# Kernel tuning notes

Hardware: AMD Instinct MI355X
Metric: run time of the kernel (lower is better)

Reference implementation:

```python
import jax, jax.numpy as jnp
import numpy as np

EMB = 128
EA = 32
ET = 32
N = 50000
E = 500000
EPS = 1e-5
DROP_P = 0.1


def setup_inputs() -> dict:
    key = jax.random.key(0)
    ks = jax.random.split(key, 12)
    din = EMB + EA + ET
    return {
        "hidden": jax.random.normal(ks[0], (N, EMB), jnp.float32),
        "edge_index": jax.random.randint(ks[1], (2, E), 0, N, jnp.int64 if jax.config.jax_enable_x64 else jnp.int32),
        "edge_attr": jax.random.normal(ks[2], (E, EA), jnp.float32),
        "edge_time_emb": jax.random.normal(ks[3], (E, ET), jnp.float32),
        "boundary_condition": jax.random.normal(ks[4], (N, EMB), jnp.float32),
        # learned params (torch Linear stored transposed: [in, out])
        "W_msg": jax.random.normal(ks[5], (din, EMB), jnp.float32) / np.sqrt(din),
        "b_msg": jnp.zeros((EMB,), jnp.float32),
        "W_lin": jax.random.normal(ks[6], (EMB, EMB), jnp.float32) / np.sqrt(EMB),
        "b_lin": jnp.zeros((EMB,), jnp.float32),
        "ln_gamma": jnp.ones((EMB,), jnp.float32),
        "ln_beta": jnp.zeros((EMB,), jnp.float32),
    }


def reference(hidden, edge_index, edge_attr, edge_time_emb, boundary_condition,
              W_msg, b_msg, W_lin, b_lin, ln_gamma, ln_beta):
    num_nodes = hidden.shape[0]
    # gather source node features, concat with edge features -> [E, emb+ea+et]
    msg = jnp.concatenate([hidden[edge_index[0]], edge_attr, edge_time_emb], axis=1)
    msg = jax.nn.relu(msg @ W_msg + b_msg)                      # [E, emb]
    # append boundary condition as self-loop messages
    msg_aug = jnp.concatenate([msg, boundary_condition], axis=0)
    idx_aug = jnp.concatenate([edge_index[1], jnp.arange(num_nodes, dtype=edge_index.dtype)])
    out = jax.ops.segment_sum(msg_aug, idx_aug, num_segments=num_nodes)  # scatter-sum [N, emb]
    out = out @ W_lin + b_lin
    # LayerNorm (eps=1e-5, affine)
    mean = out.mean(-1, keepdims=True)
    var = out.var(-1, keepdims=True)
    out = (out - mean) * jax.lax.rsqrt(var + EPS) * ln_gamma + ln_beta
    out = jax.nn.relu(out)
    # dropout p=0.1, training=True (fixed key for reproducibility)
    keep = jax.random.bernoulli(jax.random.key(42), 1.0 - DROP_P, out.shape)
    out = jnp.where(keep, out / (1.0 - DROP_P), 0.0)
    return out
```

## Files before the change

kernel.cpp:

```cpp
#include <hip/hip_runtime.h>
#include <stdint.h>

#define NN 50000
#define NE 500000
#define NEPAD 500032
#define SPB 64
#define NT_BLOCKS ((NN + 63) / 64)
#define DEG_STRIDE (NT_BLOCKS * 256)
#define NBLK_N ((NN + 255) / 256)

typedef short bf16x8 __attribute__((ext_vector_type(8)));
typedef float f32x4 __attribute__((ext_vector_type(4)));
typedef unsigned short u16;
typedef unsigned short u16x4 __attribute__((ext_vector_type(4)));
typedef unsigned short u16x8 __attribute__((ext_vector_type(8)));
typedef unsigned int u32x4 __attribute__((ext_vector_type(4)));

__device__ __forceinline__ u16 f2b(float x) {
  uint32_t u = __builtin_bit_cast(uint32_t, x);
  return (u16)((u + 0x7fffu + ((u >> 16) & 1u)) >> 16);
}
__device__ __forceinline__ float b2f(uint32_t lo16) {
  return __builtin_bit_cast(float, lo16 << 16);
}

__device__ __forceinline__ void threefry(uint32_t x0, uint32_t x1,
                                         uint32_t& o0, uint32_t& o1) {
  const uint32_t k0 = 0u, k1 = 42u, k2 = 0u ^ 42u ^ 0x1BD11BDAu;
  x0 += k0; x1 += k1;
#define TFR(r) { x0 += x1; x1 = (x1 << r) | (x1 >> (32 - r)); x1 ^= x0; }
  TFR(13) TFR(15) TFR(26) TFR(6)
  x0 += k1; x1 += k2 + 1u;
  TFR(17) TFR(29) TFR(16) TFR(24)
  x0 += k2; x1 += k0 + 2u;
  TFR(13) TFR(15) TFR(26) TFR(6)
  x0 += k0; x1 += k1 + 3u;
  TFR(17) TFR(29) TFR(16) TFR(24)
  x0 += k1; x1 += k2 + 4u;
  TFR(13) TFR(15) TFR(26) TFR(6)
  x0 += k2; x1 += k0 + 5u;
#undef TFR
  o0 = x0; o1 = x1;
}

__device__ __forceinline__ bool jax_keep(uint32_t j) {
  uint32_t o0, o1;
  threefry(0u, j, o0, o1);
  uint32_t bits = o0 ^ o1;
  float u = __builtin_bit_cast(float, (bits >> 9) | 0x3f800000u) - 1.0f;
  return u < 0.9f;
}

__global__ __launch_bounds__(256) void k_prep(const float* __restrict__ Wmsg,
                                              const float* __restrict__ Wlin,
                                              u16* __restrict__ WhImg,
                                              u16* __restrict__ WcImg,
                                              u16* __restrict__ WlImg) {
  const int t = threadIdx.x, b = blockIdx.x;
  if (b == 0) {
#pragma unroll
    for (int it = 0; it < 16; ++it) {
      int g = t + (it << 8);
      int d = g >> 5, k4 = (g & 31) << 2;
      u16x4 v = {f2b(Wmsg[(k4 + 0) * 128 + d]), f2b(Wmsg[(k4 + 1) * 128 + d]),
                 f2b(Wmsg[(k4 + 2) * 128 + d]), f2b(Wmsg[(k4 + 3) * 128 + d])};
      *(u16x4*)&WhImg[(d << 7) + k4] = v;
    }
  } else if (b == 1) {
#pragma unroll
    for (int it = 0; it < 8; ++it) {
      int g = t + (it << 8);
      int d = g >> 4, k4 = (g & 15) << 2;
      u16x4 v = {f2b(Wmsg[(128 + k4 + 0) * 128 + d]), f2b(Wmsg[(128 + k4 + 1) * 128 + d]),
                 f2b(Wmsg[(128 + k4 + 2) * 128 + d]), f2b(Wmsg[(128 + k4 + 3) * 128 + d])};
      *(u16x4*)&WcImg[(d << 6) + k4] = v;
    }
  } else {
#pragma unroll
    for (int it = 0; it < 16; ++it) {
      int g = t + (it << 8);
      int d = g >> 5, k4 = (g & 31) << 2;
      u16x4 v = {f2b(Wlin[(k4 + 0) * 128 + d]), f2b(Wlin[(k4 + 1) * 128 + d]),
                 f2b(Wlin[(k4 + 2) * 128 + d]), f2b(Wlin[(k4 + 3) * 128 + d])};
      *(u16x4*)&WlImg[(d << 7) + k4] = v;
    }
  }
}

__global__ __launch_bounds__(256) void k_scan1(const uint32_t* __restrict__ deg,
                                               uint32_t* __restrict__ ex,
                                               uint32_t* __restrict__ bsum) {
  __shared__ uint32_t s[256];
  int t = threadIdx.x;
  int i = blockIdx.x * 256 + t;
  uint32_t v = (i < NN) ? deg[i] : 0u;
  s[t] = v;
  __syncthreads();
#pragma unroll
  for (int off = 1; off < 256; off <<= 1) {
    uint32_t y = (t >= off) ? s[t - off] : 0u;
    __syncthreads();
    s[t] += y;
    __syncthreads();
  }
  if (i < NN) ex[i] = s[t] - v;
  if (t == 255) bsum[blockIdx.x] = s[255];
}

__global__ __launch_bounds__(256) void k_scan2(const uint32_t* __restrict__ bsum,
                                               uint32_t* __restrict__ boff) {
  __shared__ uint32_t s[256];
  int t = threadIdx.x;
  uint32_t v = (t < NBLK_N) ? bsum[t] : 0u;
  s[t] = v;
  __syncthreads();
#pragma unroll
  for (int off = 1; off < 256; off <<= 1) {
    uint32_t y = (t >= off) ? s[t - off] : 0u;
    __syncthreads();
    s[t] += y;
    __syncthreads();
  }
  boff[t] = s[t] - v;
}

__global__ __launch_bounds__(256) void k_scan3(const uint32_t* __restrict__ ex,
                                               const uint32_t* __restrict__ boff,
                                               uint32_t* __restrict__ cursor) {
  int i = blockIdx.x * 256 + threadIdx.x;
  if (i < NN) cursor[i] = ex[i] + boff[blockIdx.x];
}

__global__ __launch_bounds__(256) void k_permconv(const int* __restrict__ ei,
                                                  const float* __restrict__ attr,
                                                  const float* __restrict__ tim,
                                                  uint32_t* __restrict__ cursor,
                                                  u16* __restrict__ Abf,
                                                  int* __restrict__ perm) {
  const int t = threadIdx.x;
  const int j = t & 7;
  const long e = (long)blockIdx.x * 32 + (t >> 3);
  if (e >= NE) return;
  const float* src8 = (j < 4) ? (attr + ((size_t)e << 5) + (j << 3))
                              : (tim + ((size_t)e << 5) + ((j - 4) << 3));
  f32x4 v0 = *(const f32x4*)src8;
  f32x4 v1 = *(const f32x4*)(src8 + 4);
  u16x8 b = {f2b(v0[0]), f2b(v0[1]), f2b(v0[2]), f2b(v0[3]),
             f2b(v1[0]), f2b(v1[1]), f2b(v1[2]), f2b(v1[3])};
  *(u16x8*)&Abf[((size_t)e << 6) + (j << 3)] = b;
  if (j == 0) {
    uint32_t dst = (uint32_t)ei[NE + e];
    uint32_t pos = atomicAdd(&cursor[dst], 1u);
    perm[pos] = (int)e;
  }
}

__global__ __launch_bounds__(256, 4) void k_edge3(const int* __restrict__ perm,
                                                  const u16* __restrict__ Abf,
                                                  const int* __restrict__ ei,
                                                  const u16* __restrict__ WcImg,
                                                  const u16* __restrict__ Hp,
                                                  float* __restrict__ acc) {
  __shared__ union { u16 A[64 * 64]; float C[64 * 128]; } lds;
  __shared__ int sdst[64];
  const int t = threadIdx.x;
  const long e0 = (long)blockIdx.x << 6;

#pragma unroll
  for (int it = 0; it < 2; ++it) {
    int li = t + (it << 8);
    int row = li >> 3, g = li & 7;
    long sg = e0 + row;
    u32x4 v = {0u, 0u, 0u, 0u};
    if (sg < NE) {
      int e = perm[sg];
      v = *(const u32x4*)(Abf + ((size_t)e << 6) + (g << 3));
    }
    *(u32x4*)&lds.A[(row << 6) + ((g ^ (row & 7)) << 3)] = v;
  }
  const int s = t >> 2, q = t & 3;
  const long sg1 = e0 + s;
  const bool v1 = sg1 < NE;
  int src = 0, dstn = -1;
  if (v1) {
    int e = perm[sg1];
    src = ei[e];
    dstn = ei[NE + e];
  }
  u32x4 hp[4];
  if (v1) {
    const u32x4* hp4 = (const u32x4*)(Hp + ((size_t)src << 7) + (q << 5));
#pragma unroll
    for (int g = 0; g < 4; ++g) hp[g] = hp4[g];
  }
  if (q == 0) sdst[s] = v1 ? dstn : -1;
  __syncthreads();

  const int lane = t & 63, w = t >> 6;
  const int quad = lane >> 4, lr = lane & 15;
  f32x4 c[4][2];
#pragma unroll
  for (int i = 0; i < 4; ++i)
#pragma unroll
    for (int j = 0; j < 2; ++j) { f32x4 z = {0.f, 0.f, 0.f, 0.f}; c[i][j] = z; }
#pragma unroll
  for (int ks = 0; ks < 64; ks += 32) {
    const int gi = (ks >> 3) + quad;
    bf16x8 a[4], b[2];
#pragma unroll
    for (int i = 0; i < 4; ++i) {
      int row = (i << 4) + lr;
      a[i] = *(const bf16x8*)&lds.A[(row << 6) + ((gi ^ (row & 7)) << 3)];
    }
#pragma unroll
    for (int j = 0; j < 2; ++j) {
      int col = (w << 5) + (j << 4) + lr;
      b[j] = *(const bf16x8*)&WcImg[(col << 6) + (gi << 3)];
    }
#pragma unroll
    for (int i = 0; i < 4; ++i)
#pragma unroll
      for (int j = 0; j < 2; ++j)
        c[i][j] = __builtin_amdgcn_mfma_f32_16x16x32_bf16(a[i], b[j], c[i][j], 0, 0, 0);
  }
  __syncthreads();
#pragma unroll
  for (int i = 0; i < 4; ++i)
#pragma unroll
    for (int j = 0; j < 2; ++j)
#pragma unroll
      for (int r = 0; r < 4; ++r) {
        int row = (i << 4) + (quad << 2) + r;
        int col = (w << 5) + (j << 4) + lr;
        lds.C[(row << 7) + ((((col >> 2) ^ (row & 31)) << 2) + (col & 3))] = c[i][j][r];
      }
  __syncthreads();
  if (v1) {
#pragma unroll
    for (int g = 0; g < 8; ++g) {
      int cb = (q << 5) + (g << 2);
      float* p = &lds.C[(s << 7) + ((((cb >> 2) ^ (s & 31)) << 2))];
      f32x4 cv = *(const f32x4*)p;
      uint32_t w0 = hp[g >> 1][(g & 1) << 1];
      uint32_t w1 = hp[g >> 1][((g & 1) << 1) + 1];
      cv[0] = fmaxf(cv[0] + b2f(w0 & 0xffffu), 0.f);
      cv[1] = fmaxf(cv[1] + b2f(w0 >> 16), 0.f);
      cv[2] = fmaxf(cv[2] + b2f(w1 & 0xffffu), 0.f);
      cv[3] = fmaxf(cv[3] + b2f(w1 >> 16), 0.f);
      *(f32x4*)p = cv;
    }
  }
  __syncthreads();
  {
    const int col = t & 127, half = t >> 7;
    const int beg = half << 5, end = beg + 32;
    int cur = sdst[beg];
    float sum = 0.f;
    int runstart = beg;
    for (int ss = beg; ss < end; ++ss) {
      int d = sdst[ss];
      if (d != cur) {
        if (cur >= 0) {
          float* p = acc + ((size_t)cur << 7) + col;
          if (runstart == beg) unsafeAtomicAdd(p, sum);
          else *p = sum;
        }
        cur = d; sum = 0.f; runstart = ss;
      }
      sum += lds.C[(ss << 7) + ((((col >> 2) ^ (ss & 31)) << 2) + (col & 3))];
    }
    if (cur >= 0) unsafeAtomicAdd(acc + ((size_t)cur << 7) + col, sum);
  }
}

__global__ __launch_bounds__(256) void k_hp(const float* __restrict__ hidden,
                                            const u16* __restrict__ WhImg,
                                            const float* __restrict__ bmsg,
                                            const int* __restrict__ ei,
                                            uint32_t* __restrict__ deg,
                                            u16* __restrict__ Hp) {
  __shared__ u16 sA[64 * 128];
  const int t = threadIdx.x;
  const int row0 = blockIdx.x << 6;
  for (int i = blockIdx.x * 256 + t; i < NE; i += DEG_STRIDE)
    atomicAdd(&deg[ei[NE + i]], 1u);
#pragma unroll
  for (int it = 0; it < 8; ++it) {
    int li = t + (it << 8);
    int row = li >> 5, c4 = li & 31;
    int n = row0 + row;
    f32x4 v = {0.f, 0.f, 0.f, 0.f};
    if (n < NN) v = *(const f32x4*)(hidden + ((size_t)n << 7) + (c4 << 2));
    u16x4 b = {f2b(v[0]), f2b(v[1]), f2b(v[2]), f2b(v[3])};
    *(u16x4*)&sA[(row << 7) + ((((c4 >> 1) ^ (row & 15)) << 3) + ((c4 & 1) << 2))] = b;
  }
  __syncthreads();
  const int lane = t & 63, w = t >> 6;
  const int quad = lane >> 4, lr = lane & 15;
  f32x4 c[4][2];
#pragma unroll
  for (int i = 0; i < 4; ++i)
#pragma unroll
    for (int j = 0; j < 2; ++j) { f32x4 z = {0.f, 0.f, 0.f, 0.f}; c[i][j] = z; }
#pragma unroll
  for (int ks = 0; ks < 128; ks += 32) {
    const int gi = (ks >> 3) + quad;
    bf16x8 a[4], b[2];
#pragma unroll
    for (int i = 0; i < 4; ++i) {
      int row = (i << 4) + lr;
      a[i] = *(const bf16x8*)&sA[(row << 7) + ((gi ^ (row & 15)) << 3)];
    }
#pragma unroll
    for (int j = 0; j < 2; ++j) {
      int col = (w << 5) + (j << 4) + lr;
      b[j] = *(const bf16x8*)&WhImg[(col << 7) + (gi << 3)];
    }
#pragma unroll
    for (int i = 0; i < 4; ++i)
#pragma unroll
      for (int j = 0; j < 2; ++j)
        c[i][j] = __builtin_amdgcn_mfma_f32_16x16x32_bf16(a[i], b[j], c[i][j], 0, 0, 0);
  }
#pragma unroll
  for (int j = 0; j < 2; ++j) {
    int d = (w << 5) + (j << 4) + lr;
    float bias = bmsg[d];
#pragma unroll
    for (int i = 0; i < 4; ++i) {
      int nb = row0 + (i << 4) + (quad << 2);
#pragma unroll
      for (int r = 0; r < 4; ++r) {
        int n = nb + r;
        if (n < NN) Hp[((size_t)n << 7) + d] = f2b(c[i][j][r] + bias);
      }
    }
  }
}

__global__ __launch_bounds__(256) void k_out(float* accout,
                                             const float* __restrict__ bnd,
                                             const u16* __restrict__ WlImg,
                                             const float* __restrict__ blin,
                                             const float* __restrict__ gam,
                                             const float* __restrict__ bet) {
  __shared__ union { u16 A[64 * 128]; float C[64 * 128]; } lds;
  const int t = threadIdx.x;
  const int row0 = blockIdx.x << 6;
#pragma unroll
  for (int it = 0; it < 8; ++it) {
    int li = t + (it << 8);
    int row = li >> 5, c4 = li & 31;
    int n = row0 + row;
    f32x4 v = {0.f, 0.f, 0.f, 0.f};
    if (n < NN) {
      f32x4 a = *(const f32x4*)(accout + ((size_t)n << 7) + (c4 << 2));
      f32x4 b = *(const f32x4*)(bnd + ((size_t)n << 7) + (c4 << 2));
      v = a + b;
    }
    u16x4 bb = {f2b(v[0]), f2b(v[1]), f2b(v[2]), f2b(v[3])};
    *(u16x4*)&lds.A[(row << 7) + ((((c4 >> 1) ^ (row & 15)) << 3) + ((c4 & 1) << 2))] = bb;
  }
  __syncthreads();
  const int lane = t & 63, w = t >> 6;
  const int quad = lane >> 4, lr = lane & 15;
  f32x4 c[4][2];
#pragma unroll
  for (int i = 0; i < 4; ++i)
#pragma unroll
    for (int j = 0; j < 2; ++j) { f32x4 z = {0.f, 0.f, 0.f, 0.f}; c[i][j] = z; }
#pragma unroll
  for (int ks = 0; ks < 128; ks += 32) {
    const int gi = (ks >> 3) + quad;
    bf16x8 a[4], b[2];
#pragma unroll
    for (int i = 0; i < 4; ++i) {
      int row = (i << 4) + lr;
      a[i] = *(const bf16x8*)&lds.A[(row << 7) + ((gi ^ (row & 15)) << 3)];
    }
#pragma unroll
    for (int j = 0; j < 2; ++j) {
      int col = (w << 5) + (j << 4) + lr;
      b[j] = *(const bf16x8*)&WlImg[(col << 7) + (gi << 3)];
    }
#pragma unroll
    for (int i = 0; i < 4; ++i)
#pragma unroll
      for (int j = 0; j < 2; ++j)
        c[i][j] = __builtin_amdgcn_mfma_f32_16x16x32_bf16(a[i], b[j], c[i][j], 0, 0, 0);
  }
  __syncthreads();
#pragma unroll
  for (int i = 0; i < 4; ++i)
#pragma unroll
    for (int j = 0; j < 2; ++j)
#pragma unroll
      for (int r = 0; r < 4; ++r) {
        int row = (i << 4) + (quad << 2) + r;
        int col = (w << 5) + (j << 4) + lr;
        lds.C[(row << 7) + ((((col >> 2) ^ (row & 31)) << 2) + (col & 3))] = c[i][j][r];
      }
  __syncthreads();
  const int row = t >> 2, q = t & 3;
  const int n = row0 + row;
  float s1 = 0.f, s2 = 0.f;
  if (n < NN) {
#pragma unroll
    for (int g = 0; g < 8; ++g) {
      int g5 = (q << 3) + g;
      f32x4 cv = *(const f32x4*)&lds.C[(row << 7) + ((g5 ^ (row & 31)) << 2)];
      f32x4 bl = *(const f32x4*)(blin + (g5 << 2));
#pragma unroll
      for (int m = 0; m < 4; ++m) {
        float x = cv[m] + bl[m];
        s1 += x; s2 += x * x;
      }
    }
  }
  s1 += __shfl_xor(s1, 1, 64); s1 += __shfl_xor(s1, 2, 64);
  s2 += __shfl_xor(s2, 1, 64); s2 += __shfl_xor(s2, 2, 64);
  if (n < NN) {
    const float mean = s1 * 0.0078125f;
    const float var = s2 * 0.0078125f - mean * mean;
    const float inv = 1.0f / sqrtf(var + 1e-5f);
#pragma unroll
    for (int g = 0; g < 8; ++g) {
      int g5 = (q << 3) + g;
      int d0 = g5 << 2;
      f32x4 cv = *(const f32x4*)&lds.C[(row << 7) + ((g5 ^ (row & 31)) << 2)];
      f32x4 bl = *(const f32x4*)(blin + d0);
      f32x4 gm = *(const f32x4*)(gam + d0);
      f32x4 bb = *(const f32x4*)(bet + d0);
      f32x4 o;
#pragma unroll
      for (int m = 0; m < 4; ++m) {
        float x = cv[m] + bl[m];
        float y = fmaxf((x - mean) * inv * gm[m] + bb[m], 0.f);
        uint32_t jj = ((uint32_t)n << 7) + (uint32_t)(d0 + m);
        o[m] = jax_keep(jj) ? (y * (1.0f / 0.9f)) : 0.0f;
      }
      *(f32x4*)(accout + ((size_t)n << 7) + d0) = o;
    }
  }
}

extern "C" void kernel_launch(void* const* d_in, const int* in_sizes, int n_in,
                              void* d_out, int out_size, void* d_ws, size_t ws_size,
                              hipStream_t stream) {
  (void)in_sizes; (void)n_in; (void)out_size; (void)ws_size;
  const float* hidden = (const float*)d_in[0];
  const int*   ei     = (const int*)d_in[1];
  const float* attr   = (const float*)d_in[2];
  const float* tim    = (const float*)d_in[3];
  const float* bnd    = (const float*)d_in[4];
  const float* Wmsg   = (const float*)d_in[5];
  const float* bmsg   = (const float*)d_in[6];
  const float* Wlin   = (const float*)d_in[7];
  const float* blin   = (const float*)d_in[8];
  const float* gam    = (const float*)d_in[9];
  const float* bet    = (const float*)d_in[10];

  float* acc = (float*)d_out;

  char* ws = (char*)d_ws;
  u16*      Hp     = (u16*)(ws + 0);
  u16*      WhImg  = (u16*)(ws + 12800000);
  u16*      WcImg  = (u16*)(ws + 12832768);
  u16*      WlImg  = (u16*)(ws + 12849152);
  uint32_t* deg    = (uint32_t*)(ws + 12881920);
  uint32_t* cursor = (uint32_t*)(ws + 13081920);
  uint32_t* bsum   = (uint32_t*)(ws + 13281920);
  uint32_t* boff   = (uint32_t*)(ws + 13282944);
  uint32_t* ex     = (uint32_t*)(ws + 13283968);
  int*      perm   = (int*)(ws + 13483968);
  u16*      Abf    = (u16*)(ws + 15484096);

  hipMemsetAsync(deg, 0, (size_t)NN * 4, stream);
  hipMemsetAsync(acc, 0, (size_t)NN * 128 * 4, stream);

  k_prep <<<dim3(3), dim3(256), 0, stream>>>(Wmsg, Wlin, WhImg, WcImg, WlImg);
  k_hp   <<<dim3(NT_BLOCKS), dim3(256), 0, stream>>>(hidden, WhImg, bmsg, ei, deg, Hp);
  k_scan1<<<dim3(NBLK_N), dim3(256), 0, stream>>>(deg, ex, bsum);
  k_scan2<<<dim3(1), dim3(256), 0, stream>>>(bsum, boff);
  k_scan3<<<dim3(NBLK_N), dim3(256), 0, stream>>>(ex, boff, cursor);
  k_permconv<<<dim3(NE / 32), dim3(256), 0, stream>>>(ei, attr, tim, cursor, Abf, perm);
  k_edge3<<<dim3(NEPAD / SPB), dim3(256), 0, stream>>>(perm, Abf, ei, WcImg, Hp, acc);
  k_out  <<<dim3(NT_BLOCKS), dim3(256), 0, stream>>>(acc, bnd, WlImg, blin, gam, bet);
}
```

Baseline: 373.3 us.

## Drop bf16 edge-feature staging; gather fp32 attrs directly and pack src/dst per sorted slot

Removes the intermediate bf16 copy of the edge attribute and time features. The edge kernel now gathers the fp32 features through the permutation and converts them in registers, saving one full write and read pass over the edge features. The permutation kernel also stores a packed 16-bit src/dst pair per sorted slot, which replaces the dependent perm-then-edge_index lookups. The epilogue LDS buffer is halved by writing and reducing the 128 output columns in two halves, which should allow more blocks per CU but adds extra barriers and makes the fp32 gathers scattered instead of streaming.

```diff
diff --git a/kernel.cpp b/kernel.cpp
--- a/kernel.cpp
+++ b/kernel.cpp
@@ -131,37 +131,27 @@
   if (i < NN) cursor[i] = ex[i] + boff[blockIdx.x];
 }
 
-__global__ __launch_bounds__(256) void k_permconv(const int* __restrict__ ei,
+__global__ __launch_bounds__(256) void k_perm(const int* __restrict__ ei,
+                                              uint32_t* __restrict__ cursor,
+                                              int* __restrict__ perm,
+                                              uint32_t* __restrict__ sd) {
+  int i = blockIdx.x * 256 + threadIdx.x;
+  if (i < NE) {
+    uint32_t s = (uint32_t)ei[i], d = (uint32_t)ei[NE + i];
+    uint32_t pos = atomicAdd(&cursor[d], 1u);
+    perm[pos] = i;
+    sd[pos] = s | (d << 16);
+  }
+}
+
+__global__ __launch_bounds__(256, 4) void k_edge3(const int* __restrict__ perm,
+                                                  const uint32_t* __restrict__ sd,
                                                   const float* __restrict__ attr,
                                                   const float* __restrict__ tim,
-                                                  uint32_t* __restrict__ cursor,
-                                                  u16* __restrict__ Abf,
-                                                  int* __restrict__ perm) {
-  const int t = threadIdx.x;
-  const int j = t & 7;
-  const long e = (long)blockIdx.x * 32 + (t >> 3);
-  if (e >= NE) return;
-  const float* src8 = (j < 4) ? (attr + ((size_t)e << 5) + (j << 3))
-                              : (tim + ((size_t)e << 5) + ((j - 4) << 3));
-  f32x4 v0 = *(const f32x4*)src8;
-  f32x4 v1 = *(const f32x4*)(src8 + 4);
-  u16x8 b = {f2b(v0[0]), f2b(v0[1]), f2b(v0[2]), f2b(v0[3]),
-             f2b(v1[0]), f2b(v1[1]), f2b(v1[2]), f2b(v1[3])};
-  *(u16x8*)&Abf[((size_t)e << 6) + (j << 3)] = b;
-  if (j == 0) {
-    uint32_t dst = (uint32_t)ei[NE + e];
-    uint32_t pos = atomicAdd(&cursor[dst], 1u);
-    perm[pos] = (int)e;
-  }
-}
-
-__global__ __launch_bounds__(256, 4) void k_edge3(const int* __restrict__ perm,
-                                                  const u16* __restrict__ Abf,
-                                                  const int* __restrict__ ei,
                                                   const u16* __restrict__ WcImg,
                                                   const u16* __restrict__ Hp,
                                                   float* __restrict__ acc) {
-  __shared__ union { u16 A[64 * 64]; float C[64 * 128]; } lds;
+  __shared__ union { u16 A[64 * 64]; float C[64 * 64]; } lds;
   __shared__ int sdst[64];
   const int t = threadIdx.x;
   const long e0 = (long)blockIdx.x << 6;
@@ -171,27 +161,37 @@
     int li = t + (it << 8);
     int row = li >> 3, g = li & 7;
     long sg = e0 + row;
-    u32x4 v = {0u, 0u, 0u, 0u};
-    if (sg < NE) {
-      int e = perm[sg];
-      v = *(const u32x4*)(Abf + ((size_t)e << 6) + (g << 3));
-    }
-    *(u32x4*)&lds.A[(row << 6) + ((g ^ (row & 7)) << 3)] = v;
+    const bool vld = sg < NE;
+    int e = 0;
+    if (vld) e = perm[sg];
+    const float* src8 = (g < 4) ? (attr + ((size_t)e << 5) + (g << 3))
+                                : (tim + ((size_t)e << 5) + ((g - 4) << 3));
+    f32x4 v0 = {0.f, 0.f, 0.f, 0.f}, v1 = {0.f, 0.f, 0.f, 0.f};
+    if (vld) {
+      v0 = *(const f32x4*)src8;
+      v1 = *(const f32x4*)(src8 + 4);
+    }
+    u16x8 b = {f2b(v0[0]), f2b(v0[1]), f2b(v0[2]), f2b(v0[3]),
+               f2b(v1[0]), f2b(v1[1]), f2b(v1[2]), f2b(v1[3])};
+    *(u16x8*)&lds.A[(row << 6) + ((g ^ (row & 7)) << 3)] = b;
   }
   const int s = t >> 2, q = t & 3;
   const long sg1 = e0 + s;
   const bool v1 = sg1 < NE;
   int src = 0, dstn = -1;
   if (v1) {
-    int e = perm[sg1];
-    src = ei[e];
-    dstn = ei[NE + e];
+    uint32_t sdv = sd[sg1];
+    src = (int)(sdv & 0xffffu);
+    dstn = (int)(sdv >> 16);
   }
   u32x4 hp[4];
   if (v1) {
-    const u32x4* hp4 = (const u32x4*)(Hp + ((size_t)src << 7) + (q << 5));
-#pragma unroll
-    for (int g = 0; g < 4; ++g) hp[g] = hp4[g];
+#pragma unroll
+    for (int h = 0; h < 2; ++h)
+#pragma unroll
+      for (int k = 0; k < 2; ++k)
+        hp[(h << 1) + k] =
+            *(const u32x4*)(Hp + ((size_t)src << 7) + (h << 6) + (q << 4) + (k << 3));
   }
   if (q == 0) sdst[s] = v1 ? dstn : -1;
   __syncthreads();
@@ -224,52 +224,62 @@
         c[i][j] = __builtin_amdgcn_mfma_f32_16x16x32_bf16(a[i], b[j], c[i][j], 0, 0, 0);
   }
   __syncthreads();
-#pragma unroll
-  for (int i = 0; i < 4; ++i)
-#pragma unroll
-    for (int j = 0; j < 2; ++j)
-#pragma unroll
-      for (int r = 0; r < 4; ++r) {
-        int row = (i << 4) + (quad << 2) + r;
-        int col = (w << 5) + (j << 4) + lr;
-        lds.C[(row << 7) + ((((col >> 2) ^ (row & 31)) << 2) + (col & 3))] = c[i][j][r];
-      }
-  __syncthreads();
-  if (v1) {
-#pragma unroll
-    for (int g = 0; g < 8; ++g) {
-      int cb = (q << 5) + (g << 2);
-      float* p = &lds.C[(s << 7) + ((((cb >> 2) ^ (s & 31)) << 2))];
-      f32x4 cv = *(const f32x4*)p;
-      uint32_t w0 = hp[g >> 1][(g & 1) << 1];
-      uint32_t w1 = hp[g >> 1][((g & 1) << 1) + 1];
-      cv[0] = fmaxf(cv[0] + b2f(w0 & 0xffffu), 0.f);
-      cv[1] = fmaxf(cv[1] + b2f(w0 >> 16), 0.f);
-      cv[2] = fmaxf(cv[2] + b2f(w1 & 0xffffu), 0.f);
-      cv[3] = fmaxf(cv[3] + b2f(w1 >> 16), 0.f);
-      *(f32x4*)p = cv;
-    }
-  }
-  __syncthreads();
-  {
-    const int col = t & 127, half = t >> 7;
-    const int beg = half << 5, end = beg + 32;
-    int cur = sdst[beg];
-    float sum = 0.f;
-    int runstart = beg;
-    for (int ss = beg; ss < end; ++ss) {
-      int d = sdst[ss];
-      if (d != cur) {
-        if (cur >= 0) {
-          float* p = acc + ((size_t)cur << 7) + col;
-          if (runstart == beg) unsafeAtomicAdd(p, sum);
-          else *p = sum;
+
+#pragma unroll
+  for (int h = 0; h < 2; ++h) {
+    if ((w >> 1) == h) {
+#pragma unroll
+      for (int i = 0; i < 4; ++i)
+#pragma unroll
+        for (int j = 0; j < 2; ++j)
+#pragma unroll
+          for (int r = 0; r < 4; ++r) {
+            int row = (i << 4) + (quad << 2) + r;
+            int colh = ((w & 1) << 5) + (j << 4) + lr;
+            lds.C[(row << 6) + ((((colh >> 2) ^ (row & 15)) << 2) + (colh & 3))] =
+                c[i][j][r];
+          }
+    }
+    __syncthreads();
+    if (v1) {
+      const u32x4 h0 = hp[h << 1], h1 = hp[(h << 1) + 1];
+#pragma unroll
+      for (int g = 0; g < 4; ++g) {
+        int cb = (q << 4) + (g << 2);
+        float* p = &lds.C[(s << 6) + (((cb >> 2) ^ (s & 15)) << 2)];
+        f32x4 cv = *(const f32x4*)p;
+        u32x4 hw = (g < 2) ? h0 : h1;
+        uint32_t w0 = hw[(g & 1) << 1];
+        uint32_t w1 = hw[((g & 1) << 1) + 1];
+        cv[0] = fmaxf(cv[0] + b2f(w0 & 0xffffu), 0.f);
+        cv[1] = fmaxf(cv[1] + b2f(w0 >> 16), 0.f);
+        cv[2] = fmaxf(cv[2] + b2f(w1 & 0xffffu), 0.f);
+        cv[3] = fmaxf(cv[3] + b2f(w1 >> 16), 0.f);
+        *(f32x4*)p = cv;
+      }
+    }
+    __syncthreads();
+    {
+      const int col = t & 63, rng = t >> 6;
+      const int beg = rng << 4, end = beg + 16;
+      int cur = sdst[beg];
+      float sum = 0.f;
+      int runstart = beg;
+      for (int ss = beg; ss < end; ++ss) {
+        int d = sdst[ss];
+        if (d != cur) {
+          if (cur >= 0) {
+            float* p = acc + ((size_t)cur << 7) + (h << 6) + col;
+            if (runstart == beg) unsafeAtomicAdd(p, sum);
+            else *p = sum;
+          }
+          cur = d; sum = 0.f; runstart = ss;
         }
-        cur = d; sum = 0.f; runstart = ss;
-      }
-      sum += lds.C[(ss << 7) + ((((col >> 2) ^ (ss & 31)) << 2) + (col & 3))];
-    }
-    if (cur >= 0) unsafeAtomicAdd(acc + ((size_t)cur << 7) + col, sum);
+        sum += lds.C[(ss << 6) + ((((col >> 2) ^ (ss & 15)) << 2) + (col & 3))];
+      }
+      if (cur >= 0) unsafeAtomicAdd(acc + ((size_t)cur << 7) + (h << 6) + col, sum);
+    }
+    __syncthreads();
   }
 }
 
@@ -472,8 +482,8 @@
   uint32_t* bsum   = (uint32_t*)(ws + 13281920);
   uint32_t* boff   = (uint32_t*)(ws + 13282944);
   uint32_t* ex     = (uint32_t*)(ws + 13283968);
-  int*      perm   = (int*)(ws + 13483968);
-  u16*      Abf    = (u16*)(ws + 15484096);
+  uint32_t* sd     = (uint32_t*)(ws + 13483968);
+  int*      perm   = (int*)(ws + 15484096);
 
   hipMemsetAsync(deg, 0, (size_t)NN * 4, stream);
   hipMemsetAsync(acc, 0, (size_t)NN * 128 * 4, stream);
@@ -483,7 +493,7 @@
   k_scan1<<<dim3(NBLK_N), dim3(256), 0, stream>>>(deg, ex, bsum);
   k_scan2<<<dim3(1), dim3(256), 0, stream>>>(bsum, boff);
   k_scan3<<<dim3(NBLK_N), dim3(256), 0, stream>>>(ex, boff, cursor);
-  k_permconv<<<dim3(NE / 32), dim3(256), 0, stream>>>(ei, attr, tim, cursor, Abf, perm);
-  k_edge3<<<dim3(NEPAD / SPB), dim3(256), 0, stream>>>(perm, Abf, ei, WcImg, Hp, acc);
+  k_perm <<<dim3((NE + 255) / 256), dim3(256), 0, stream>>>(ei, cursor, perm, sd);
+  k_edge3<<<dim3(NEPAD / SPB), dim3(256), 0, stream>>>(perm, sd, attr, tim, WcImg, Hp, acc);
   k_out  <<<dim3(NT_BLOCKS), dim3(256), 0, stream>>>(acc, bnd, WlImg, blin, gam, bet);
 }
```

After: 362.8 us. 2.8% less time.

## Gather fp32 edge features directly in persistent edge kernel with register prefetch

Applied to the files above, without the earlier changes.

Removes the intermediate bf16 edge-feature buffer. The permute kernel now only builds perm plus packed src/dst, and the edge kernel gathers fp32 attr/time rows through perm and converts them to bf16 in-kernel. The edge kernel becomes persistent over a fixed grid and prefetches the next tile's features into registers while the current tile computes. This saves writing and re-reading a 64 MB bf16 copy, at the cost of scattered fp32 reads of twice the bytes, more registers, and a packing that assumes node ids fit in 16 bits.

```diff
diff --git a/kernel.cpp b/kernel.cpp
--- a/kernel.cpp
+++ b/kernel.cpp
@@ -4,7 +4,8 @@
 #define NN 50000
 #define NE 500000
 #define NEPAD 500032
-#define SPB 64
+#define NTILES (NEPAD / 64)
+#define EGRID 1024
 #define NT_BLOCKS ((NN + 63) / 64)
 #define DEG_STRIDE (NT_BLOCKS * 256)
 #define NBLK_N ((NN + 255) / 256)
@@ -23,6 +24,12 @@
 __device__ __forceinline__ float b2f(uint32_t lo16) {
   return __builtin_bit_cast(float, lo16 << 16);
 }
+
+#define EBAR()                                            \
+  {                                                       \
+    asm volatile("s_waitcnt lgkmcnt(0)" ::: "memory");    \
+    __builtin_amdgcn_s_barrier();                         \
+  }
 
 __device__ __forceinline__ void threefry(uint32_t x0, uint32_t x1,
                                          uint32_t& o0, uint32_t& o1) {
@@ -131,145 +138,182 @@
   if (i < NN) cursor[i] = ex[i] + boff[blockIdx.x];
 }
 
-__global__ __launch_bounds__(256) void k_permconv(const int* __restrict__ ei,
+__global__ __launch_bounds__(256) void k_perm(const int* __restrict__ ei,
+                                              uint32_t* __restrict__ cursor,
+                                              int* __restrict__ perm,
+                                              uint32_t* __restrict__ sd) {
+  int i = blockIdx.x * 256 + threadIdx.x;
+  if (i < NE) {
+    uint32_t s = (uint32_t)ei[i], d = (uint32_t)ei[NE + i];
+    uint32_t pos = atomicAdd(&cursor[d], 1u);
+    perm[pos] = i;
+    sd[pos] = s | (d << 16);
+  }
+}
+
+struct Pf {
+  f32x4 a00, a01, a10, a11;
+  uint32_t sdv;
+  int dst;
+  bool v1;
+};
+
+__device__ __forceinline__ void pf_issue_a(Pf& p, long e0, int t,
+                                           const int* __restrict__ perm,
+                                           const uint32_t* __restrict__ sd,
+                                           const float* __restrict__ attr,
+                                           const float* __restrict__ tim) {
+  const int row = t >> 3, g = t & 7;
+  long sg0 = e0 + row, sg1 = e0 + row + 32;
+  int ea = perm[sg0 < NE ? sg0 : 0];
+  int eb = perm[sg1 < NE ? sg1 : 0];
+  const float* pa = (g < 4) ? attr + ((size_t)ea << 5) + (g << 3)
+                            : tim + ((size_t)ea << 5) + ((g & 3) << 3);
+  const float* pb = (g < 4) ? attr + ((size_t)eb << 5) + (g << 3)
+                            : tim + ((size_t)eb << 5) + ((g & 3) << 3);
+  p.a00 = *(const f32x4*)pa;
+  p.a01 = *(const f32x4*)(pa + 4);
+  p.a10 = *(const f32x4*)pb;
+  p.a11 = *(const f32x4*)(pb + 4);
+  const int s = t >> 2;
+  long sgs = e0 + s;
+  p.v1 = sgs < NE;
+  p.sdv = sd[p.v1 ? sgs : 0];
+  p.dst = p.v1 ? (int)(p.sdv >> 16) : -1;
+}
+
+__device__ __forceinline__ void pf_write_a(const Pf& p, int t,
+                                           u16* __restrict__ A,
+                                           int* __restrict__ sdst) {
+  const int row = t >> 3, g = t & 7;
+  u16x8 b0 = {f2b(p.a00[0]), f2b(p.a00[1]), f2b(p.a00[2]), f2b(p.a00[3]),
+              f2b(p.a01[0]), f2b(p.a01[1]), f2b(p.a01[2]), f2b(p.a01[3])};
+  *(u16x8*)&A[(row << 6) + ((g ^ (row & 7)) << 3)] = b0;
+  const int row1 = row + 32;
+  u16x8 b1 = {f2b(p.a10[0]), f2b(p.a10[1]), f2b(p.a10[2]), f2b(p.a10[3]),
+              f2b(p.a11[0]), f2b(p.a11[1]), f2b(p.a11[2]), f2b(p.a11[3])};
+  *(u16x8*)&A[(row1 << 6) + ((g ^ (row1 & 7)) << 3)] = b1;
+  if ((t & 3) == 0) sdst[t >> 2] = p.dst;
+}
+
+__global__ __launch_bounds__(256, 4) void k_edge3(const int* __restrict__ perm,
+                                                  const uint32_t* __restrict__ sd,
                                                   const float* __restrict__ attr,
                                                   const float* __restrict__ tim,
-                                                  uint32_t* __restrict__ cursor,
-                                                  u16* __restrict__ Abf,
-                                                  int* __restrict__ perm) {
-  const int t = threadIdx.x;
-  const int j = t & 7;
-  const long e = (long)blockIdx.x * 32 + (t >> 3);
-  if (e >= NE) return;
-  const float* src8 = (j < 4) ? (attr + ((size_t)e << 5) + (j << 3))
-                              : (tim + ((size_t)e << 5) + ((j - 4) << 3));
-  f32x4 v0 = *(const f32x4*)src8;
-  f32x4 v1 = *(const f32x4*)(src8 + 4);
-  u16x8 b = {f2b(v0[0]), f2b(v0[1]), f2b(v0[2]), f2b(v0[3]),
-             f2b(v1[0]), f2b(v1[1]), f2b(v1[2]), f2b(v1[3])};
-  *(u16x8*)&Abf[((size_t)e << 6) + (j << 3)] = b;
-  if (j == 0) {
-    uint32_t dst = (uint32_t)ei[NE + e];
-    uint32_t pos = atomicAdd(&cursor[dst], 1u);
-    perm[pos] = (int)e;
-  }
-}
-
-__global__ __launch_bounds__(256, 4) void k_edge3(const int* __restrict__ perm,
-                                                  const u16* __restrict__ Abf,
-                                                  const int* __restrict__ ei,
                                                   const u16* __restrict__ WcImg,
                                                   const u16* __restrict__ Hp,
                                                   float* __restrict__ acc) {
   __shared__ union { u16 A[64 * 64]; float C[64 * 128]; } lds;
   __shared__ int sdst[64];
   const int t = threadIdx.x;
-  const long e0 = (long)blockIdx.x << 6;
-
-#pragma unroll
-  for (int it = 0; it < 2; ++it) {
-    int li = t + (it << 8);
-    int row = li >> 3, g = li & 7;
-    long sg = e0 + row;
-    u32x4 v = {0u, 0u, 0u, 0u};
-    if (sg < NE) {
-      int e = perm[sg];
-      v = *(const u32x4*)(Abf + ((size_t)e << 6) + (g << 3));
-    }
-    *(u32x4*)&lds.A[(row << 6) + ((g ^ (row & 7)) << 3)] = v;
-  }
-  const int s = t >> 2, q = t & 3;
-  const long sg1 = e0 + s;
-  const bool v1 = sg1 < NE;
-  int src = 0, dstn = -1;
-  if (v1) {
-    int e = perm[sg1];
-    src = ei[e];
-    dstn = ei[NE + e];
-  }
-  u32x4 hp[4];
-  if (v1) {
-    const u32x4* hp4 = (const u32x4*)(Hp + ((size_t)src << 7) + (q << 5));
-#pragma unroll
-    for (int g = 0; g < 4; ++g) hp[g] = hp4[g];
-  }
-  if (q == 0) sdst[s] = v1 ? dstn : -1;
-  __syncthreads();
-
   const int lane = t & 63, w = t >> 6;
   const int quad = lane >> 4, lr = lane & 15;
-  f32x4 c[4][2];
-#pragma unroll
-  for (int i = 0; i < 4; ++i)
-#pragma unroll
-    for (int j = 0; j < 2; ++j) { f32x4 z = {0.f, 0.f, 0.f, 0.f}; c[i][j] = z; }
-#pragma unroll
-  for (int ks = 0; ks < 64; ks += 32) {
-    const int gi = (ks >> 3) + quad;
-    bf16x8 a[4], b[2];
-#pragma unroll
-    for (int i = 0; i < 4; ++i) {
-      int row = (i << 4) + lr;
-      a[i] = *(const bf16x8*)&lds.A[(row << 6) + ((gi ^ (row & 7)) << 3)];
-    }
-#pragma unroll
-    for (int j = 0; j < 2; ++j) {
-      int col = (w << 5) + (j << 4) + lr;
-      b[j] = *(const bf16x8*)&WcImg[(col << 6) + (gi << 3)];
-    }
+  const int s = t >> 2, q = t & 3;
+
+  int tile = blockIdx.x;
+  Pf pf;
+  pf_issue_a(pf, (long)tile << 6, t, perm, sd, attr, tim);
+
+  while (true) {
+    const int ntile = tile + EGRID;
+    const bool more = ntile < NTILES;
+
+    pf_write_a(pf, t, lds.A, sdst);
+    Pf pf2;
+    if (more) pf_issue_a(pf2, (long)ntile << 6, t, perm, sd, attr, tim);
+
+    const int src = pf.v1 ? (int)(pf.sdv & 0xffffu) : 0;
+    const u32x4* hp4 = (const u32x4*)(Hp + ((size_t)src << 7) + (q << 5));
+    u32x4 h0 = hp4[0], h1 = hp4[1], h2 = hp4[2], h3 = hp4[3];
+
+    EBAR();
+
+    f32x4 c[4][2];
 #pragma unroll
     for (int i = 0; i < 4; ++i)
 #pragma unroll
+      for (int j = 0; j < 2; ++j) { f32x4 z = {0.f, 0.f, 0.f, 0.f}; c[i][j] = z; }
+#pragma unroll
+    for (int ks = 0; ks < 64; ks += 32) {
+      const int gi = (ks >> 3) + quad;
+      bf16x8 a[4], b[2];
+#pragma unroll
+      for (int i = 0; i < 4; ++i) {
+        int row = (i << 4) + lr;
+        a[i] = *(const bf16x8*)&lds.A[(row << 6) + ((gi ^ (row & 7)) << 3)];
+      }
+#pragma unroll
+      for (int j = 0; j < 2; ++j) {
+        int col = (w << 5) + (j << 4) + lr;
+        b[j] = *(const bf16x8*)&WcImg[(col << 6) + (gi << 3)];
+      }
+#pragma unroll
+      for (int i = 0; i < 4; ++i)
+#pragma unroll
+        for (int j = 0; j < 2; ++j)
+          c[i][j] = __builtin_amdgcn_mfma_f32_16x16x32_bf16(a[i], b[j], c[i][j], 0, 0, 0);
+    }
+
+    EBAR();
+
+#pragma unroll
+    for (int i = 0; i < 4; ++i)
+#pragma unroll
       for (int j = 0; j < 2; ++j)
-        c[i][j] = __builtin_amdgcn_mfma_f32_16x16x32_bf16(a[i], b[j], c[i][j], 0, 0, 0);
-  }
-  __syncthreads();
-#pragma unroll
-  for (int i = 0; i < 4; ++i)
-#pragma unroll
-    for (int j = 0; j < 2; ++j)
-#pragma unroll
-      for (int r = 0; r < 4; ++r) {
-        int row = (i << 4) + (quad << 2) + r;
-        int col = (w << 5) + (j << 4) + lr;
-        lds.C[(row << 7) + ((((col >> 2) ^ (row & 31)) << 2) + (col & 3))] = c[i][j][r];
-      }
-  __syncthreads();
-  if (v1) {
-#pragma unroll
-    for (int g = 0; g < 8; ++g) {
-      int cb = (q << 5) + (g << 2);
-      float* p = &lds.C[(s << 7) + ((((cb >> 2) ^ (s & 31)) << 2))];
-      f32x4 cv = *(const f32x4*)p;
-      uint32_t w0 = hp[g >> 1][(g & 1) << 1];
-      uint32_t w1 = hp[g >> 1][((g & 1) << 1) + 1];
-      cv[0] = fmaxf(cv[0] + b2f(w0 & 0xffffu), 0.f);
-      cv[1] = fmaxf(cv[1] + b2f(w0 >> 16), 0.f);
-      cv[2] = fmaxf(cv[2] + b2f(w1 & 0xffffu), 0.f);
-      cv[3] = fmaxf(cv[3] + b2f(w1 >> 16), 0.f);
-      *(f32x4*)p = cv;
-    }
-  }
-  __syncthreads();
-  {
-    const int col = t & 127, half = t >> 7;
-    const int beg = half << 5, end = beg + 32;
-    int cur = sdst[beg];
-    float sum = 0.f;
-    int runstart = beg;
-    for (int ss = beg; ss < end; ++ss) {
-      int d = sdst[ss];
-      if (d != cur) {
-        if (cur >= 0) {
-          float* p = acc + ((size_t)cur << 7) + col;
-          if (runstart == beg) unsafeAtomicAdd(p, sum);
-          else *p = sum;
+#pragma unroll
+        for (int r = 0; r < 4; ++r) {
+          int row = (i << 4) + (quad << 2) + r;
+          int col = (w << 5) + (j << 4) + lr;
+          lds.C[(row << 7) + ((((col >> 2) ^ (row & 31)) << 2) + (col & 3))] = c[i][j][r];
         }
-        cur = d; sum = 0.f; runstart = ss;
-      }
-      sum += lds.C[(ss << 7) + ((((col >> 2) ^ (ss & 31)) << 2) + (col & 3))];
-    }
-    if (cur >= 0) unsafeAtomicAdd(acc + ((size_t)cur << 7) + col, sum);
+
+    EBAR();
+
+    if (pf.v1) {
+#pragma unroll
+      for (int g = 0; g < 8; ++g) {
+        const u32x4 hw = (g < 2) ? h0 : (g < 4) ? h1 : (g < 6) ? h2 : h3;
+        int cb = (q << 5) + (g << 2);
+        float* p = &lds.C[(s << 7) + ((((cb >> 2) ^ (s & 31)) << 2))];
+        f32x4 cv = *(const f32x4*)p;
+        uint32_t w0 = hw[(g & 1) << 1];
+        uint32_t w1 = hw[((g & 1) << 1) + 1];
+        cv[0] = fmaxf(cv[0] + b2f(w0 & 0xffffu), 0.f);
+        cv[1] = fmaxf(cv[1] + b2f(w0 >> 16), 0.f);
+        cv[2] = fmaxf(cv[2] + b2f(w1 & 0xffffu), 0.f);
+        cv[3] = fmaxf(cv[3] + b2f(w1 >> 16), 0.f);
+        *(f32x4*)p = cv;
+      }
+    }
+
+    EBAR();
+
+    {
+      const int col = t & 127, half = t >> 7;
+      const int beg = half << 5, end = beg + 32;
+      int cur = sdst[beg];
+      float sum = 0.f;
+      int runstart = beg;
+      for (int ss = beg; ss < end; ++ss) {
+        int d = sdst[ss];
+        if (d != cur) {
+          if (cur >= 0) {
+            float* p = acc + ((size_t)cur << 7) + col;
+            if (runstart == beg) unsafeAtomicAdd(p, sum);
+            else *p = sum;
+          }
+          cur = d; sum = 0.f; runstart = ss;
+        }
+        sum += lds.C[(ss << 7) + ((((col >> 2) ^ (ss & 31)) << 2) + (col & 3))];
+      }
+      if (cur >= 0) unsafeAtomicAdd(acc + ((size_t)cur << 7) + col, sum);
+    }
+
+    EBAR();
+
+    if (!more) break;
+    pf = pf2;
+    tile = ntile;
   }
 }
 
@@ -472,8 +516,8 @@
   uint32_t* bsum   = (uint32_t*)(ws + 13281920);
   uint32_t* boff   = (uint32_t*)(ws + 13282944);
   uint32_t* ex     = (uint32_t*)(ws + 13283968);
-  int*      perm   = (int*)(ws + 13483968);
-  u16*      Abf    = (u16*)(ws + 15484096);
+  uint32_t* sd     = (uint32_t*)(ws + 13483968);
+  int*      perm   = (int*)(ws + 15484096);
 
   hipMemsetAsync(deg, 0, (size_t)NN * 4, stream);
   hipMemsetAsync(acc, 0, (size_t)NN * 128 * 4, stream);
@@ -483,7 +527,7 @@
   k_scan1<<<dim3(NBLK_N), dim3(256), 0, stream>>>(deg, ex, bsum);
   k_scan2<<<dim3(1), dim3(256), 0, stream>>>(bsum, boff);
   k_scan3<<<dim3(NBLK_N), dim3(256), 0, stream>>>(ex, boff, cursor);
-  k_permconv<<<dim3(NE / 32), dim3(256), 0, stream>>>(ei, attr, tim, cursor, Abf, perm);
-  k_edge3<<<dim3(NEPAD / SPB), dim3(256), 0, stream>>>(perm, Abf, ei, WcImg, Hp, acc);
+  k_perm <<<dim3((NE + 255) / 256), dim3(256), 0, stream>>>(ei, cursor, perm, sd);
+  k_edge3<<<dim3(EGRID), dim3(256), 0, stream>>>(perm, sd, attr, tim, WcImg, Hp, acc);
   k_out  <<<dim3(NT_BLOCKS), dim3(256), 0, stream>>>(acc, bnd, WlImg, blin, gam, bet);
 }
```

New measurement: 429.7 us. +15.1%, slower.
